# Performance work log

Measured on AMD Instinct MI355X. Metric: run time of the kernel, lower is better.

## Reference

```python
import jax, jax.numpy as jnp
import numpy as np

RATE = 2
KSIZE = 3          # patch size for similarity
KERNEL = 2 * RATE  # patch size for alpha scatter (4)
BN_EPS = 1e-5


def _extract_patches(x, k, s):
    """Mirror of GuidedCxtAtten.extract_patches: reflect-pad then unfold.
    x: [B,C,H,W] -> [B,Ho,Wo,C,k,k] with Ho=H//s, Wo=W//s."""
    left = (k - s + 1) // 2
    right = (k - s) // 2
    xp = jnp.pad(x, ((0, 0), (0, 0), (left, right), (left, right)), mode='reflect')
    Hp, Wp = xp.shape[2], xp.shape[3]
    Ho = (Hp - k) // s + 1
    Wo = (Wp - k) // s + 1
    ii = (jnp.arange(Ho) * s)[:, None] + jnp.arange(k)[None, :]   # [Ho,k]
    jj = (jnp.arange(Wo) * s)[:, None] + jnp.arange(k)[None, :]   # [Wo,k]
    p = xp[:, :, ii[:, :, None, None], jj[None, None, :, :]]      # [B,C,Ho,k,Wo,k]
    return p.transpose(0, 2, 4, 1, 3, 5)                          # [B,Ho,Wo,C,k,k]


def setup_inputs() -> dict:
    key = jax.random.key(0)
    ks = jax.random.split(key, 5)
    B, Cg, Ca, H, W = 4, 256, 128, 128, 128
    f = jax.random.normal(ks[0], (B, Cg, H, W), dtype=jnp.float32)
    alpha = jax.random.normal(ks[1], (B, Ca, H, W), dtype=jnp.float32)
    unknown = (jax.random.uniform(ks[2], (B, 1, H, W)) > 0.5).astype(jnp.float32)
    # guidance_conv: 1x1, Cg -> Cg//2, xavier-ish
    gc_w = jax.random.normal(ks[3], (Cg // 2, Cg), dtype=jnp.float32) * np.sqrt(2.0 / (Cg + Cg // 2))
    gc_b = jnp.zeros((Cg // 2,), dtype=jnp.float32)
    # W[0]: 1x1 conv Ca->Ca no bias; W[1]: BN with gamma=0.001, beta=0 per init
    w_w = jax.random.normal(ks[4], (Ca, Ca), dtype=jnp.float32) * np.sqrt(1.0 / Ca)
    bn_gamma = jnp.full((Ca,), 0.001, dtype=jnp.float32)
    bn_beta = jnp.zeros((Ca,), dtype=jnp.float32)
    return {"f": f, "alpha": alpha, "unknown": unknown, "gc_w": gc_w, "gc_b": gc_b,
            "w_w": w_w, "bn_gamma": bn_gamma, "bn_beta": bn_beta}


def _forward(f, alpha, unknown, gc_w, gc_b, w_w, bn_gamma, bn_beta):
    # guidance 1x1 conv
    fg = jnp.einsum('oi,bihw->bohw', gc_w, f) + gc_b[None, :, None, None]
    B, _, H, W = fg.shape
    Ca = alpha.shape[1]
    Hs, Ws = H // RATE, W // RATE
    L = Hs * Ws

    # alpha patches [B,L,Ca,4,4] (kernel=2*rate, stride=rate)
    alpha_w = _extract_patches(alpha, KERNEL, RATE).reshape(B, L, Ca, KERNEL, KERNEL)

    # nearest downsample by rate (torch nearest with scale 1/2 == strided pick)
    f_ds = fg[:, :, ::RATE, ::RATE]                # [B,Cg/2,Hs,Ws]
    unk_ds = unknown[:, :, ::RATE, ::RATE]         # [B,1,Hs,Ws]

    # similarity filter patches [B,L,C,3,3]
    w = _extract_patches(f_ds, KSIZE, 1).reshape(B, L, -1, KSIZE, KSIZE)

    # known/unknown softmax scales [B,2]
    u_mean = unk_ds.mean(axis=(2, 3))              # [B,1]
    k_mean = 1.0 - u_mean
    su = jnp.clip(jnp.sqrt(u_mean / k_mean), 0.1, 10.0)
    sk = jnp.clip(jnp.sqrt(k_mean / u_mean), 0.1, 10.0)
    softmax_scale = jnp.concatenate([su, sk], axis=1)

    # patch-mean of unknown mask -> binary patch mask [B,L]
    m = _extract_patches(unk_ds, KSIZE, 1).reshape(B, L, -1).mean(axis=2)
    mm = (m > 0.0).astype(fg.dtype)

    # l2-normalize filters per patch, then correlate against all positions.
    # Conv of reflect-padded f_ds with stride-1 3x3 patch filters == inner
    # product of normalized patches with the raw patches (same extraction).
    norm = jnp.sqrt(jnp.sum(w * w, axis=(2, 3, 4), keepdims=True))
    w_normed = w / jnp.maximum(norm, 1e-4)
    scores = jnp.einsum('bqcij,bpcij->bqp', w_normed, w)   # [B,L(q=patch),L(p=pos)]

    # known/unknown scaling per source patch q
    gate = jnp.where(mm > 0.0, su, sk)                      # [B,L]
    scores = scores * gate[:, :, None]

    # self-match suppression only for unknown patches (diagonal q == p)
    diag = jnp.arange(L)
    scores = scores.at[:, diag, diag].add(-10000.0 * mm)

    attn = jax.nn.softmax(scores, axis=1)                   # softmax over patches q

    # offsets (argmax patch per position, relative to center)
    idx = jnp.argmax(attn, axis=1)                          # [B,L]
    offsets = jnp.stack([idx // Ws, idx % Ws], axis=1).reshape(B, 2, Hs, Ws)
    offsets = offsets - jnp.array([Hs // 2, Ws // 2]).reshape(1, 2, 1, 1)

    # scatter alpha patches with attention weights: per-sample conv_transpose2d
    attn_map = attn.reshape(B, L, Hs, Ws)

    def ct(yi, wc):  # yi [L,Hs,Ws], wc [L,Ca,4,4]
        rhs = jnp.flip(wc, (2, 3)).transpose(1, 0, 2, 3)    # [Ca,L,4,4]
        pad = KERNEL - 1 - 1                                # torch padding=1
        out = jax.lax.conv_general_dilated(
            yi[None], rhs, window_strides=(1, 1),
            padding=[(pad, pad), (pad, pad)], lhs_dilation=(RATE, RATE),
            dimension_numbers=('NCHW', 'OIHW', 'NCHW'))
        return out[0]

    y = jax.vmap(ct)(attn_map, alpha_w) / 4.0               # [B,Ca,H,W]

    # W: 1x1 conv (no bias) + BatchNorm2d (training-mode batch stats)
    yw = jnp.einsum('oi,bihw->bohw', w_w, y)
    mean = yw.mean(axis=(0, 2, 3))
    var = yw.var(axis=(0, 2, 3))
    yn = (yw - mean[None, :, None, None]) * jax.lax.rsqrt(var + BN_EPS)[None, :, None, None]
    yn = yn * bn_gamma[None, :, None, None] + bn_beta[None, :, None, None]

    return yn + alpha, offsets, softmax_scale


def reference(f, alpha, unknown, gc_w, gc_b, w_w, bn_gamma, bn_beta):
    return _forward(f, alpha, unknown, gc_w, gc_b, w_w, bn_gamma, bn_beta)
```

## Files before the change

kernel.cpp:

```cpp
#include <hip/hip_runtime.h>
#include <math.h>

#define B 4
#define CG 256
#define CM 128
#define CA 128
#define H 128
#define W_ 128
#define HS 64
#define WS 64
#define L 4096
#define D1 1152
#define D2 2048
#define NPIX 65536
#define NT1 36
#define NT2 128

#define STP_F 8388608UL
#define RA_F  4194304UL
#define SLOT_F (STP_F + RA_F + RA_F)

typedef unsigned short u16;
typedef __attribute__((ext_vector_type(8))) short short8v;
typedef __attribute__((ext_vector_type(4))) unsigned short u16x4;
typedef __attribute__((ext_vector_type(4))) float f32x4;

__device__ __forceinline__ float bf2f(u16 x) {
    union { unsigned int u; float f; } v; v.u = ((unsigned int)x) << 16; return v.f;
}
__device__ __forceinline__ u16 f2bf(float x) {
    union { float f; unsigned int u; } v; v.f = x;
    unsigned int r = (v.u + 0x7FFFu + ((v.u >> 16) & 1u)) >> 16;
    return (u16)r;
}
__device__ __forceinline__ void gll16(const void* g, void* l) {
    __builtin_amdgcn_global_load_lds((const __attribute__((address_space(1))) void*)g,
                                     (__attribute__((address_space(3))) void*)l, 16, 0, 0);
}
__device__ __forceinline__ int refl(int i, int n) {
    return i < 0 ? -i : (i >= n ? 2 * n - 2 - i : i);
}
__device__ __forceinline__ int swz(int row, int fq) {
    return row * 32 + ((fq ^ ((row >> 1) & 3)) * 8);
}
__device__ __forceinline__ short8v rdfrag32(const char* lds, int r, int fq) {
    return *(const short8v*)(lds + r * 64 + ((fq * 16) ^ (((r >> 1) & 3) << 4)));
}

__global__ __launch_bounds__(256) void k_conv_ds(const float* __restrict__ f,
                                                 const float* __restrict__ gw,
                                                 const float* __restrict__ gb,
                                                 float* __restrict__ fds,
                                                 float* __restrict__ ssq) {
    __shared__ float sf[CG * 64];
    __shared__ float part[4][64];
    int t = threadIdx.x;
    int hs = blockIdx.x, b = blockIdx.y;
    const float* fb = f + (size_t)b * CG * H * W_ + (2 * hs) * W_;
    for (int idx = t; idx < CG * 64; idx += 256) {
        int ci = idx >> 6, ws = idx & 63;
        sf[idx] = fb[(size_t)ci * H * W_ + 2 * ws];
    }
    __syncthreads();
    int ws = t & 63;
    int wave = __builtin_amdgcn_readfirstlane(t >> 6);
    const float* gwp = gw + (size_t)(wave * 32) * CG;
    float acc[32];
#pragma unroll
    for (int r = 0; r < 32; ++r) acc[r] = gb[wave * 32 + r];
    for (int ci = 0; ci < CG; ++ci) {
        float fv = sf[ci * 64 + ws];
#pragma unroll
        for (int r = 0; r < 32; ++r) acc[r] += gwp[r * CG + ci] * fv;
    }
    float sq = 0.f;
#pragma unroll
    for (int r = 0; r < 32; ++r) {
        int co = wave * 32 + r;
        fds[(((size_t)b * CM + co) * HS + hs) * WS + ws] = acc[r];
        sq += acc[r] * acc[r];
    }
    part[wave][ws] = sq;
    __syncthreads();
    if (t < 64)
        ssq[((size_t)b * HS + hs) * WS + t] =
            part[0][t] + part[1][t] + part[2][t] + part[3][t];
}

__global__ __launch_bounds__(256) void k_scale(const float* __restrict__ unk,
                                               float* __restrict__ suk,
                                               float* __restrict__ out2) {
    int b = blockIdx.x, t = threadIdx.x;
    __shared__ float red[256];
    float s = 0.f;
    for (int i = t; i < L; i += 256) {
        int hs = i >> 6, ws = i & 63;
        s += unk[(size_t)b * H * W_ + (2 * hs) * W_ + 2 * ws];
    }
    red[t] = s;
    __syncthreads();
    for (int o = 128; o > 0; o >>= 1) {
        if (t < o) red[t] += red[t + o];
        __syncthreads();
    }
    if (t == 0) {
        float u = red[0] / (float)L;
        float k = 1.0f - u;
        float su = sqrtf(u / k); su = fminf(fmaxf(su, 0.1f), 10.0f);
        float sk = sqrtf(k / u); sk = fminf(fmaxf(sk, 0.1f), 10.0f);
        suk[b * 2] = su; suk[b * 2 + 1] = sk;
        out2[b * 2] = su; out2[b * 2 + 1] = sk;
    }
}

__global__ __launch_bounds__(64) void k_gate(const float* __restrict__ unk,
                                             const float* __restrict__ ssq,
                                             const float* __restrict__ suk,
                                             float* __restrict__ g,
                                             float* __restrict__ dg) {
    int ws = threadIdx.x, hs = blockIdx.x, b = blockIdx.y;
    float sm = 0.f, sq = 0.f;
    for (int di = -1; di <= 1; ++di) {
        int rh = refl(hs + di, HS);
        for (int dj = -1; dj <= 1; ++dj) {
            int rw = refl(ws + dj, WS);
            sm += unk[(size_t)b * H * W_ + (2 * rh) * W_ + 2 * rw];
            sq += ssq[((size_t)b * HS + rh) * WS + rw];
        }
    }
    float mm   = (sm > 0.0f) ? 1.0f : 0.0f;
    float norm = sqrtf(sq);
    float gate = (mm > 0.0f) ? suk[2 * b] : suk[2 * b + 1];
    int q = hs * WS + ws;
    g[(size_t)b * L + q]  = gate / fmaxf(norm, 1e-4f);
    dg[(size_t)b * L + q] = -10000.0f * mm;
}

__global__ __launch_bounds__(256) void k_buildW(const float* __restrict__ fds,
                                                float* __restrict__ base, int b0) {
    int bz = blockIdx.z;
    int b  = b0 + bz;
    u16* Whi = (u16*)(base + (size_t)bz * SLOT_F + STP_F);
    int ws = threadIdx.x;
    int c  = blockIdx.y * 4 + threadIdx.y;
    int hs = blockIdx.x;
    int q = hs * WS + ws;
    size_t bo = (size_t)q * D1 + c * 9;
    const float* src = fds + ((size_t)b * CM + c) * HS * WS;
#pragma unroll
    for (int i = 0; i < 3; ++i) {
        int rh = refl(hs + i - 1, HS);
#pragma unroll
        for (int j = 0; j < 3; ++j) {
            int rw = refl(ws + j - 1, WS);
            Whi[bo + i * 3 + j] = f2bf(src[rh * WS + rw]);
        }
    }
}

__global__ __launch_bounds__(256, 3) void k_gemm1(float* __restrict__ base,
                                                  const float* __restrict__ g0,
                                                  const float* __restrict__ dg0,
                                                  int b0) {
    __shared__ u16 sA[3][128 * 32], sB[3][128 * 32];
    int bz = blockIdx.z;
    float* S = base + (size_t)bz * SLOT_F;
    u16* STP = (u16*)S;
    const u16* Whi = (const u16*)(S + STP_F);
    const float* g  = g0  + (size_t)(b0 + bz) * L;
    const float* dg = dg0 + (size_t)(b0 + bz) * L;

    int tid = threadIdx.x;
    int wv = tid >> 6, lane = tid & 63;
    int t0 = blockIdx.x, I = 0;
    while (t0 >= 32 - I) { t0 -= 32 - I; ++I; }
    int J = I + t0;
    int pTile = I * 128, qTile = J * 128;
    int wp = (wv >> 1) * 64, wq = (wv & 1) * 64;
    int r0 = wv * 32;
    int lrow = lane >> 2;
    int csw = ((lane & 3) ^ ((lrow >> 1) & 3)) * 8;
    int fr = lane & 15, fq = lane >> 4;

    const u16* gArow = Whi + (size_t)(pTile + r0 + lrow) * D1 + csw;
    const u16* gBrow = Whi + (size_t)(qTile + r0 + lrow) * D1 + csw;

#define G1STG(kt, bf) do { \
    gll16(gArow + (kt) * 32, &sA[bf][r0 * 32]); \
    gll16(gArow + (kt) * 32 + (size_t)16 * D1, &sA[bf][(r0 + 16) * 32]); \
    gll16(gBrow + (kt) * 32, &sB[bf][r0 * 32]); \
    gll16(gBrow + (kt) * 32 + (size_t)16 * D1, &sB[bf][(r0 + 16) * 32]); } while (0)

#define G1PHASE(t, ca, cb, na, nb_) do { \
    int nxb = ((t) + 1) % 3; \
    _Pragma("unroll") for (int i = 0; i < 4; ++i) \
        nb_[i] = *(const short8v*)&sB[nxb][swz(wq + i * 16 + fr, fq)]; \
    __builtin_amdgcn_s_setprio(1); \
    _Pragma("unroll") for (int mi = 0; mi < 2; ++mi) \
        _Pragma("unroll") for (int ni = 0; ni < 4; ++ni) \
            acc[mi][ni] = __builtin_amdgcn_mfma_f32_16x16x32_bf16(ca[mi], cb[ni], acc[mi][ni], 0, 0, 0); \
    __builtin_amdgcn_s_setprio(0); \
    _Pragma("unroll") for (int i = 0; i < 4; ++i) \
        na[i] = *(const short8v*)&sA[nxb][swz(wp + i * 16 + fr, fq)]; \
    G1STG(((t) + 3 < NT1) ? (t) + 3 : 0, (t) % 3); \
    asm volatile("s_waitcnt vmcnt(4)" ::: "memory"); \
    __builtin_amdgcn_s_setprio(1); \
    _Pragma("unroll") for (int mi = 2; mi < 4; ++mi) \
        _Pragma("unroll") for (int ni = 0; ni < 4; ++ni) \
            acc[mi][ni] = __builtin_amdgcn_mfma_f32_16x16x32_bf16(ca[mi], cb[ni], acc[mi][ni], 0, 0, 0); \
    __builtin_amdgcn_s_setprio(0); \
    asm volatile("s_waitcnt lgkmcnt(0)" ::: "memory"); \
    __builtin_amdgcn_s_barrier(); \
    __builtin_amdgcn_sched_barrier(0); } while (0)

    f32x4 acc[4][4];
#pragma unroll
    for (int mi = 0; mi < 4; ++mi)
#pragma unroll
        for (int ni = 0; ni < 4; ++ni)
#pragma unroll
            for (int r = 0; r < 4; ++r) acc[mi][ni][r] = 0.f;

    G1STG(0, 0);
    G1STG(1, 1);
    G1STG(2, 2);
    asm volatile("s_waitcnt vmcnt(4)" ::: "memory");
    __builtin_amdgcn_s_barrier();
    __builtin_amdgcn_sched_barrier(0);

    short8v fa0[4], fb0[4], fa1[4], fb1[4];
#pragma unroll
    for (int i = 0; i < 4; ++i) {
        fa0[i] = *(const short8v*)&sA[0][swz(wp + i * 16 + fr, fq)];
        fb0[i] = *(const short8v*)&sB[0][swz(wq + i * 16 + fr, fq)];
    }
    asm volatile("s_waitcnt lgkmcnt(0)" ::: "memory");
    __builtin_amdgcn_s_barrier();
    __builtin_amdgcn_sched_barrier(0);

    for (int t = 0; t < NT1; t += 2) {
        G1PHASE(t,     fa0, fb0, fa1, fb1);
        G1PHASE(t + 1, fa1, fb1, fa0, fb0);
    }
#undef G1PHASE
#undef G1STG

#pragma unroll
    for (int ni = 0; ni < 4; ++ni) {
        int qq = qTile + wq + ni * 16 + fr;
        float gq = g[qq];
        float dq = dg[qq];
#pragma unroll
        for (int mi = 0; mi < 4; ++mi) {
            int pB = pTile + wp + mi * 16 + fq * 4;
#pragma unroll
            for (int r = 0; r < 4; ++r) {
                int p = pB + r;
                float v = acc[mi][ni][r] * gq;
                if (p == qq) v += dq;
                STP[(size_t)p * L + qq] = f2bf(v);
            }
        }
    }
    if (I != J) {
#pragma unroll
        for (int mi = 0; mi < 4; ++mi) {
            int p0 = pTile + wp + mi * 16 + fq * 4;
            float gp0 = g[p0], gp1 = g[p0 + 1], gp2 = g[p0 + 2], gp3 = g[p0 + 3];
#pragma unroll
            for (int ni = 0; ni < 4; ++ni) {
                int qq = qTile + wq + ni * 16 + fr;
                u16x4 mv;
                mv[0] = f2bf(acc[mi][ni][0] * gp0);
                mv[1] = f2bf(acc[mi][ni][1] * gp1);
                mv[2] = f2bf(acc[mi][ni][2] * gp2);
                mv[3] = f2bf(acc[mi][ni][3] * gp3);
                *(u16x4*)(STP + (size_t)qq * L + p0) = mv;
            }
        }
    }
}

__global__ __launch_bounds__(256) void k_softmax(float* __restrict__ base,
                                                 const float* __restrict__ fds,
                                                 const float* __restrict__ g0,
                                                 const float* __restrict__ dg0,
                                                 float* __restrict__ rowsum,
                                                 float* __restrict__ out1, int b0) {
    __shared__ float wmax[4], wsum[4], cred[4];
    __shared__ int candList[128];
    __shared__ int candCount;
    int bz = blockIdx.y;
    int b  = b0 + bz;
    float* S = base + (size_t)bz * SLOT_F;
    u16* STP = (u16*)S;
    const float* fdsb = fds + (size_t)b * CM * HS * WS;
    const float* g  = g0  + (size_t)b * L;
    const float* dg = dg0 + (size_t)b * L;

    int p = blockIdx.x, t = threadIdx.x;
    int lane = t & 63, wv = t >> 6;
    u16* rowp = STP + (size_t)p * L;

    if (t == 0) candCount = 0;
    float mx = -3.4e38f;
    for (int i = t; i < L / 8; i += 256) {
        short8v v8 = ((const short8v*)rowp)[i];
#pragma unroll
        for (int j = 0; j < 8; ++j) mx = fmaxf(mx, bf2f((u16)v8[j]));
    }
#pragma unroll
    for (int o = 32; o > 0; o >>= 1) mx = fmaxf(mx, __shfl_xor(mx, o));
    if (lane == 0) wmax[wv] = mx;
    __syncthreads();
    float M = fmaxf(fmaxf(wmax[0], wmax[1]), fmaxf(wmax[2], wmax[3]));
    float cth = M - (fabsf(M) * 0.0625f + 1e-5f);

    float s = 0.f;
    for (int i = t; i < L / 8; i += 256) {
        short8v v8 = ((const short8v*)rowp)[i];
        short8v o8;
#pragma unroll
        for (int j = 0; j < 8; ++j) {
            float v = bf2f((u16)v8[j]);
            if (v >= cth) {
                int ix = atomicAdd(&candCount, 1);
                if (ix < 128) candList[ix] = i * 8 + j;
            }
            float e = __expf(v - M);
            o8[j] = (short)f2bf(e);
            s += e;
        }
        ((short8v*)rowp)[i] = o8;
    }
#pragma unroll
    for (int o = 32; o > 0; o >>= 1) s += __shfl_xor(s, o);
    if (lane == 0) wsum[wv] = s;
    __syncthreads();
    if (t == 0) rowsum[(size_t)b * L + p] = wsum[0] + wsum[1] + wsum[2] + wsum[3];

    int nc = candCount; if (nc > 128) nc = 128;
    int bestI;
    if (nc == 1) {
        bestI = candList[0];
    } else {
        float bestE = -3.4e38f; bestI = L;
        int hp = p >> 6, wpp = p & 63;
        for (int k = 0; k < nc; ++k) {
            int cand = candList[k];
            int hc = cand >> 6, wcc = cand & 63;
            float part = 0.f;
#pragma unroll
            for (int e = 0; e < 5; ++e) {
                int kk = t + e * 256;
                if (kk < D1) {
                    int c  = kk / 9, ij = kk - c * 9;
                    int di = ij / 3, dj = ij - di * 3;
                    float pv = fdsb[(size_t)c * (HS * WS)
                                    + refl(hp + di - 1, HS) * WS + refl(wpp + dj - 1, WS)];
                    float cv = fdsb[(size_t)c * (HS * WS)
                                    + refl(hc + di - 1, HS) * WS + refl(wcc + dj - 1, WS)];
                    part += pv * cv;
                }
            }
#pragma unroll
            for (int o = 32; o > 0; o >>= 1) part += __shfl_xor(part, o);
            if (lane == 0) cred[wv] = part;
            __syncthreads();
            float e1 = (cred[0] + cred[1] + cred[2] + cred[3]) * g[cand]
                     + (p == cand ? dg[cand] : 0.f);
            if (e1 > bestE || (e1 == bestE && cand < bestI)) { bestE = e1; bestI = cand; }
            __syncthreads();
        }
    }
    if (t == 0) {
        out1[(size_t)(b * 2 + 0) * L + p] = (float)(bestI / WS - 32);
        out1[(size_t)(b * 2 + 1) * L + p] = (float)(bestI % WS - 32);
    }
}

__global__ __launch_bounds__(256) void k_buildA(const float* __restrict__ alpha,
                                                float* __restrict__ base, int b0) {
    int bz = blockIdx.z;
    int b  = b0 + bz;
    u16* At = (u16*)(base + (size_t)bz * SLOT_F + STP_F);
    int q0 = (blockIdx.x * 256 + threadIdx.x) * 4;
    int n  = blockIdx.y;
    int c = n & 127, kikj = n >> 7, ki = kikj >> 2, kj = kikj & 3;
    int hs = q0 >> 6, ws = q0 & 63;
    int rh = refl(2 * hs + ki - 1, H);
    const float* arow = alpha + ((size_t)b * CA + c) * H * W_ + rh * W_;
    u16x4 ov;
#pragma unroll
    for (int j = 0; j < 4; ++j)
        ov[j] = f2bf(arow[refl(2 * (ws + j) + kj - 1, W_)]);
    *(u16x4*)(At + (size_t)n * L + q0) = ov;
}

__global__ __launch_bounds__(512, 2) void k_gemm2(float* __restrict__ base) {
    __shared__ u16 smem[65536];
    char* sm = (char*)smem;
    int bz = blockIdx.z;
    float* S = base + (size_t)bz * SLOT_F;
    const u16* P  = (const u16*)S;
    const u16* At = (const u16*)(S + STP_F);
    u16* Z        = (u16*)(S + STP_F + RA_F);

    int tid = threadIdx.x;
    int wid = tid >> 6, lane = tid & 63;
    int wm = wid >> 2, wn = wid & 3;
    int pTile = blockIdx.x * 256, nTile = blockIdx.y * 256;
    int fr = lane & 15, fq = lane >> 4;

    int off0 = wid * 1024 + lane * 16;
    int row0 = off0 >> 6, cb0 = off0 & 63;
    int off1 = off0 + 8192;
    int row1 = off1 >> 6, cb1 = off1 & 63;
    const u16* pA0 = P  + (size_t)(pTile + row0) * L + ((cb0 ^ (((row0 >> 1) & 3) << 4)) >> 1);
    const u16* pA1 = P  + (size_t)(pTile + row1) * L + ((cb1 ^ (((row1 >> 1) & 3) << 4)) >> 1);
    const u16* pB0 = At + (size_t)(nTile + row0) * L + ((cb0 ^ (((row0 >> 1) & 3) << 4)) >> 1);
    const u16* pB1 = At + (size_t)(nTile + row1) * L + ((cb1 ^ (((row1 >> 1) & 3) << 4)) >> 1);

#define STG2(kt, bi) do { \
    char* d = sm + (bi) * 32768 + wid * 1024; \
    gll16(pA0 + (size_t)(kt) * 32, d); \
    gll16(pA1 + (size_t)(kt) * 32, d + 8192); \
    gll16(pB0 + (size_t)(kt) * 32, d + 16384); \
    gll16(pB1 + (size_t)(kt) * 32, d + 24576); } while (0)

#define PRELOAD2(fa, fb, bi) do { \
    const char* Ab_ = sm + (bi) * 32768; \
    const char* Bb_ = Ab_ + 16384; \
    _Pragma("unroll") for (int n = 0; n < 4; ++n) fb[n] = rdfrag32(Bb_, wn * 64 + n * 16 + fr, fq); \
    _Pragma("unroll") for (int m = 0; m < 8; ++m) fa[m] = rdfrag32(Ab_, wm * 128 + m * 16 + fr, fq); } while (0)

#define PHASE2(t, ca, cb, na, nb_) do { \
    const char* Abn = sm + (((t) + 1) & 3) * 32768; \
    const char* Bbn = Abn + 16384; \
    _Pragma("unroll") for (int n = 0; n < 4; ++n) nb_[n] = rdfrag32(Bbn, wn * 64 + n * 16 + fr, fq); \
    __builtin_amdgcn_s_setprio(1); \
    _Pragma("unroll") for (int m = 0; m < 4; ++m) \
        _Pragma("unroll") for (int n = 0; n < 4; ++n) \
            acc[m][n] = __builtin_amdgcn_mfma_f32_16x16x32_bf16(ca[m], cb[n], acc[m][n], 0, 0, 0); \
    __builtin_amdgcn_s_setprio(0); \
    _Pragma("unroll") for (int m = 0; m < 8; ++m) na[m] = rdfrag32(Abn, wm * 128 + m * 16 + fr, fq); \
    STG2(((t) + 3 < NT2) ? (t) + 3 : 0, ((t) + 3) & 3); \
    asm volatile("s_waitcnt vmcnt(4)" ::: "memory"); \
    __builtin_amdgcn_s_setprio(1); \
    _Pragma("unroll") for (int m = 4; m < 8; ++m) \
        _Pragma("unroll") for (int n = 0; n < 4; ++n) \
            acc[m][n] = __builtin_amdgcn_mfma_f32_16x16x32_bf16(ca[m], cb[n], acc[m][n], 0, 0, 0); \
    __builtin_amdgcn_s_setprio(0); \
    asm volatile("s_waitcnt lgkmcnt(0)" ::: "memory"); \
    __builtin_amdgcn_s_barrier(); \
    __builtin_amdgcn_sched_barrier(0); } while (0)

    f32x4 acc[8][4];
#pragma unroll
    for (int m = 0; m < 8; ++m)
#pragma unroll
        for (int n = 0; n < 4; ++n)
#pragma unroll
            for (int r = 0; r < 4; ++r) acc[m][n][r] = 0.f;

    STG2(0, 0);
    STG2(1, 1);
    STG2(2, 2);
    asm volatile("s_waitcnt vmcnt(4)" ::: "memory");
    __builtin_amdgcn_s_barrier();
    __builtin_amdgcn_sched_barrier(0);

    short8v fa0[8], fb0[4], fa1[8], fb1[4];
    PRELOAD2(fa0, fb0, 0);
    asm volatile("s_waitcnt lgkmcnt(0)" ::: "memory");
    __builtin_amdgcn_s_barrier();
    __builtin_amdgcn_sched_barrier(0);

    for (int t = 0; t < NT2; t += 2) {
        PHASE2(t,     fa0, fb0, fa1, fb1);
        PHASE2(t + 1, fa1, fb1, fa0, fb0);
    }
#undef PHASE2
#undef PRELOAD2
#undef STG2

#pragma unroll
    for (int m = 0; m < 8; ++m)
#pragma unroll
        for (int n = 0; n < 4; ++n) {
            int nn = nTile + wn * 64 + n * 16 + fr;
#pragma unroll
            for (int r = 0; r < 4; ++r) {
                int pp = pTile + wm * 128 + m * 16 + fq * 4 + r;
                Z[(size_t)pp * D2 + nn] = f2bf(acc[m][n][r]);
            }
        }
}

__global__ __launch_bounds__(256) void k_gather(float* __restrict__ base,
                                                const float* __restrict__ rowsum,
                                                u16* __restrict__ yt, int b0) {
    int bz = blockIdx.z;
    int b  = b0 + bz;
    const u16* Z = (const u16*)(base + (size_t)bz * SLOT_F + STP_F + RA_F);
    const float* rs = rowsum + (size_t)b * L;
    int c  = threadIdx.x & 127;
    int pl = threadIdx.x >> 7;
    int w  = blockIdx.x * 2 + pl;
    int h  = blockIdx.y;
    float s = 0.f;
#pragma unroll
    for (int ki = 0; ki < 4; ++ki) {
        int num = h + 1 - ki;
        if (num < 0 || (num & 1)) continue;
        int hs = num >> 1;
        if (hs >= HS) continue;
#pragma unroll
        for (int kj = 0; kj < 4; ++kj) {
            int numw = w + 1 - kj;
            if (numw < 0 || (numw & 1)) continue;
            int wsd = numw >> 1;
            if (wsd >= WS) continue;
            int src = hs * WS + wsd;
            s += bf2f(Z[(size_t)src * D2 + (ki * 4 + kj) * 128 + c]) / rs[src];
        }
    }
    int pix = h * W_ + w;
    int cs = c ^ ((pix & 7) << 3);
    yt[((size_t)b * 16384 + pix) * 128 + cs] = f2bf(0.25f * s);
}

__global__ __launch_bounds__(256) void k_cvtww(const float* __restrict__ ww,
                                               u16* __restrict__ wwbf) {
    int i = blockIdx.x * 256 + threadIdx.x;
    int o = i >> 7, c = i & 127;
    wwbf[o * 128 + (c ^ ((o & 7) << 3))] = f2bf(ww[i]);
}

__global__ __launch_bounds__(256) void k_ywgemm(const u16* __restrict__ wwbf,
                                                const u16* __restrict__ yt,
                                                float* __restrict__ yw) {
    __shared__ u16 sA[128 * 128], sB[128 * 128];
    int tid = threadIdx.x;
    int wv = tid >> 6, lane = tid & 63;
    int nTile = blockIdx.x * 128;
    int wp = (wv >> 1) * 64, wn = (wv & 1) * 64;
    int fr = lane & 15, fq = lane >> 4;

    const u16* gB = yt + (size_t)nTile * 128;
#pragma unroll
    for (int i = 0; i < 8; ++i) {
        int o = (i * 4 + wv) * 512;
        gll16(wwbf + o + lane * 8, &sA[o]);
        gll16(gB + o + lane * 8, &sB[o]);
    }
    __syncthreads();

    f32x4 acc[4][4];
#pragma unroll
    for (int mi = 0; mi < 4; ++mi)
#pragma unroll
        for (int ni = 0; ni < 4; ++ni)
#pragma unroll
            for (int r = 0; r < 4; ++r) acc[mi][ni][r] = 0.f;

#pragma unroll
    for (int ks = 0; ks < 4; ++ks) {
        int k0 = ks * 32 + fq * 8;
        short8v a[4], bb[4];
#pragma unroll
        for (int i = 0; i < 4; ++i) {
            int ra = wp + i * 16 + fr;
            a[i] = *(const short8v*)&sA[ra * 128 + (k0 ^ ((ra & 7) << 3))];
            int rb = wn + i * 16 + fr;
            bb[i] = *(const short8v*)&sB[rb * 128 + (k0 ^ ((rb & 7) << 3))];
        }
#pragma unroll
        for (int mi = 0; mi < 4; ++mi)
#pragma unroll
            for (int ni = 0; ni < 4; ++ni)
                acc[mi][ni] = __builtin_amdgcn_mfma_f32_16x16x32_bf16(a[mi], bb[ni], acc[mi][ni], 0, 0, 0);
    }

#pragma unroll
    for (int mi = 0; mi < 4; ++mi)
#pragma unroll
        for (int ni = 0; ni < 4; ++ni) {
            int gp = nTile + wn + ni * 16 + fr;
#pragma unroll
            for (int r = 0; r < 4; ++r) {
                int o = wp + mi * 16 + fq * 4 + r;
                yw[(size_t)o * NPIX + gp] = acc[mi][ni][r];
            }
        }
}

__global__ __launch_bounds__(256) void k_stats(const float* __restrict__ yw,
                                               float* __restrict__ meanvar) {
    int o = blockIdx.x, t = threadIdx.x;
    __shared__ float rs[256], rq[256];
    float s = 0.f, q = 0.f;
    const float* p = yw + (size_t)o * NPIX;
    for (int i = t; i < NPIX; i += 256) {
        float v = p[i];
        s += v;
        q += v * v;
    }
    rs[t] = s; rq[t] = q;
    __syncthreads();
    for (int off = 128; off > 0; off >>= 1) {
        if (t < off) { rs[t] += rs[t + off]; rq[t] += rq[t + off]; }
        __syncthreads();
    }
    if (t == 0) {
        float n = (float)NPIX;
        float mean = rs[0] / n;
        float var  = rq[0] / n - mean * mean;
        meanvar[o] = mean;
        meanvar[CA + o] = var;
    }
}

__global__ __launch_bounds__(256) void k_final(const float* __restrict__ yw,
                                               const float* __restrict__ meanvar,
                                               const float* __restrict__ gamma,
                                               const float* __restrict__ beta,
                                               const float* __restrict__ alpha,
                                               float* __restrict__ out0) {
    size_t i = ((size_t)blockIdx.x * 256 + threadIdx.x) * 4;
    int c = (int)((i >> 14) & 127);
    int b = (int)(i >> 21);
    int pix = (int)(i & 16383);
    float4 v = *(const float4*)(yw + (size_t)c * NPIX + b * 16384 + pix);
    float4 a = *(const float4*)(alpha + i);
    float mean = meanvar[c];
    float var  = meanvar[CA + c];
    float sc   = rsqrtf(var + 1e-5f) * gamma[c];
    float bt   = beta[c];
    float4 r;
    r.x = (v.x - mean) * sc + bt + a.x;
    r.y = (v.y - mean) * sc + bt + a.y;
    r.z = (v.z - mean) * sc + bt + a.z;
    r.w = (v.w - mean) * sc + bt + a.w;
    *(float4*)(out0 + i) = r;
}

extern "C" void kernel_launch(void* const* d_in, const int* in_sizes, int n_in,
                              void* d_out, int out_size, void* d_ws, size_t ws_size,
                              hipStream_t stream) {
    (void)in_sizes; (void)n_in; (void)out_size;
    const float* f     = (const float*)d_in[0];
    const float* alpha = (const float*)d_in[1];
    const float* unk   = (const float*)d_in[2];
    const float* gw    = (const float*)d_in[3];
    const float* gb    = (const float*)d_in[4];
    const float* ww    = (const float*)d_in[5];
    const float* gamma = (const float*)d_in[6];
    const float* beta  = (const float*)d_in[7];

    float* out0 = (float*)d_out;
    float* out1 = out0 + (size_t)B * CA * H * W_;
    float* out2 = out1 + (size_t)B * 2 * HS * WS;

    float* wsf = (float*)d_ws;
    size_t off = 0;
    float* fds     = wsf + off; off += (size_t)B * CM * HS * WS;
    float* ssq     = wsf + off; off += (size_t)B * HS * WS;
    float* gbuf    = wsf + off; off += (size_t)B * L;
    float* dgbuf   = wsf + off; off += (size_t)B * L;
    float* suk     = wsf + off; off += 64;
    float* ytF     = wsf + off; off += (size_t)NPIX * 128 / 2;
    float* wwbfF   = wsf + off; off += 8192;
    float* meanvar = wsf + off; off += 256;
    float* rowsum  = wsf + off; off += (size_t)B * L;
    float* base    = wsf + off;

    const size_t PRE_F = off;
    int nb = (ws_size >= (PRE_F + 4 * SLOT_F) * sizeof(float)) ? 4 : 2;

    float* yw   = base;
    u16*   yt   = (u16*)ytF;
    u16*   wwbf = (u16*)wwbfF;

    k_cvtww<<<64, 256, 0, stream>>>(ww, wwbf);
    k_conv_ds<<<dim3(64, 4), 256, 0, stream>>>(f, gw, gb, fds, ssq);
    k_scale<<<4, 256, 0, stream>>>(unk, suk, out2);
    k_gate<<<dim3(64, 4), 64, 0, stream>>>(unk, ssq, suk, gbuf, dgbuf);

    for (int b0 = 0; b0 < B; b0 += nb) {
        k_buildW<<<dim3(64, 32, nb), dim3(64, 4), 0, stream>>>(fds, base, b0);
        k_gemm1<<<dim3(528, 1, nb), 256, 0, stream>>>(base, gbuf, dgbuf, b0);
        k_softmax<<<dim3(4096, nb), 256, 0, stream>>>(base, fds, gbuf, dgbuf, rowsum, out1, b0);
        k_buildA<<<dim3(4, 2048, nb), 256, 0, stream>>>(alpha, base, b0);
        k_gemm2<<<dim3(16, 8, nb), 512, 0, stream>>>(base);
        k_gather<<<dim3(64, 128, nb), 256, 0, stream>>>(base, rowsum, yt, b0);
    }

    k_ywgemm<<<512, 256, 0, stream>>>(wwbf, yt, yw);
    k_stats<<<128, 256, 0, stream>>>(yw, meanvar);
    k_final<<<8192, 256, 0, stream>>>(yw, meanvar, gamma, beta, alpha, out0);
}
```

Measured before the change: 803.7 us.

## Map one softmax row per wavefront and keep row in registers

The softmax/argmax kernel now gives each 64-lane wavefront its own row, so four rows run per block instead of one row per 256-thread block. Each lane loads its eight 16-byte chunks into registers once and reuses them for both the max pass and the exp pass, instead of reading global memory twice. All block-level __syncthreads and shared reductions, including those in the candidate-refinement loop, become wave-local shuffles. This raises register use and caps candidates per row at 64 instead of 128, which could change the argmax if more than 64 near-max candidates occur.

```diff
diff --git a/kernel.cpp b/kernel.cpp
--- a/kernel.cpp
+++ b/kernel.cpp
@@ -287,9 +287,8 @@
                                                  const float* __restrict__ dg0,
                                                  float* __restrict__ rowsum,
                                                  float* __restrict__ out1, int b0) {
-    __shared__ float wmax[4], wsum[4], cred[4];
-    __shared__ int candList[128];
-    __shared__ int candCount;
+    __shared__ int candList[4][64];
+    __shared__ int candCount[4];
     int bz = blockIdx.y;
     int b  = b0 + bz;
     float* S = base + (size_t)bz * SLOT_F;
@@ -298,82 +297,76 @@
     const float* g  = g0  + (size_t)b * L;
     const float* dg = dg0 + (size_t)b * L;
 
-    int p = blockIdx.x, t = threadIdx.x;
+    int t = threadIdx.x;
     int lane = t & 63, wv = t >> 6;
+    int p = blockIdx.x * 4 + wv;
     u16* rowp = STP + (size_t)p * L;
-
-    if (t == 0) candCount = 0;
+    if (lane == 0) candCount[wv] = 0;
+
+    short8v v[8];
+#pragma unroll
+    for (int j = 0; j < 8; ++j) v[j] = ((const short8v*)rowp)[j * 64 + lane];
+
     float mx = -3.4e38f;
-    for (int i = t; i < L / 8; i += 256) {
-        short8v v8 = ((const short8v*)rowp)[i];
-#pragma unroll
-        for (int j = 0; j < 8; ++j) mx = fmaxf(mx, bf2f((u16)v8[j]));
-    }
+#pragma unroll
+    for (int j = 0; j < 8; ++j)
+#pragma unroll
+        for (int jj = 0; jj < 8; ++jj) mx = fmaxf(mx, bf2f((u16)v[j][jj]));
 #pragma unroll
     for (int o = 32; o > 0; o >>= 1) mx = fmaxf(mx, __shfl_xor(mx, o));
-    if (lane == 0) wmax[wv] = mx;
-    __syncthreads();
-    float M = fmaxf(fmaxf(wmax[0], wmax[1]), fmaxf(wmax[2], wmax[3]));
+    float M = mx;
     float cth = M - (fabsf(M) * 0.0625f + 1e-5f);
 
     float s = 0.f;
-    for (int i = t; i < L / 8; i += 256) {
-        short8v v8 = ((const short8v*)rowp)[i];
+#pragma unroll
+    for (int j = 0; j < 8; ++j) {
         short8v o8;
 #pragma unroll
-        for (int j = 0; j < 8; ++j) {
-            float v = bf2f((u16)v8[j]);
-            if (v >= cth) {
-                int ix = atomicAdd(&candCount, 1);
-                if (ix < 128) candList[ix] = i * 8 + j;
+        for (int jj = 0; jj < 8; ++jj) {
+            float x = bf2f((u16)v[j][jj]);
+            if (x >= cth) {
+                int ix = atomicAdd(&candCount[wv], 1);
+                if (ix < 64) candList[wv][ix] = (j * 64 + lane) * 8 + jj;
             }
-            float e = __expf(v - M);
-            o8[j] = (short)f2bf(e);
+            float e = __expf(x - M);
+            o8[jj] = (short)f2bf(e);
             s += e;
         }
-        ((short8v*)rowp)[i] = o8;
+        ((short8v*)rowp)[j * 64 + lane] = o8;
     }
 #pragma unroll
     for (int o = 32; o > 0; o >>= 1) s += __shfl_xor(s, o);
-    if (lane == 0) wsum[wv] = s;
-    __syncthreads();
-    if (t == 0) rowsum[(size_t)b * L + p] = wsum[0] + wsum[1] + wsum[2] + wsum[3];
-
-    int nc = candCount; if (nc > 128) nc = 128;
+    if (lane == 0) rowsum[(size_t)b * L + p] = s;
+
+    int nc = candCount[wv]; if (nc > 64) nc = 64;
     int bestI;
     if (nc == 1) {
-        bestI = candList[0];
+        bestI = candList[wv][0];
     } else {
         float bestE = -3.4e38f; bestI = L;
         int hp = p >> 6, wpp = p & 63;
         for (int k = 0; k < nc; ++k) {
-            int cand = candList[k];
+            int cand = candList[wv][k];
             int hc = cand >> 6, wcc = cand & 63;
             float part = 0.f;
 #pragma unroll
-            for (int e = 0; e < 5; ++e) {
-                int kk = t + e * 256;
-                if (kk < D1) {
-                    int c  = kk / 9, ij = kk - c * 9;
-                    int di = ij / 3, dj = ij - di * 3;
-                    float pv = fdsb[(size_t)c * (HS * WS)
-                                    + refl(hp + di - 1, HS) * WS + refl(wpp + dj - 1, WS)];
-                    float cv = fdsb[(size_t)c * (HS * WS)
-                                    + refl(hc + di - 1, HS) * WS + refl(wcc + dj - 1, WS)];
-                    part += pv * cv;
-                }
+            for (int e = 0; e < 18; ++e) {
+                int kk = lane + e * 64;
+                int c  = kk / 9, ij = kk - c * 9;
+                int di = ij / 3, dj = ij - di * 3;
+                float pv = fdsb[(size_t)c * (HS * WS)
+                                + refl(hp + di - 1, HS) * WS + refl(wpp + dj - 1, WS)];
+                float cv = fdsb[(size_t)c * (HS * WS)
+                                + refl(hc + di - 1, HS) * WS + refl(wcc + dj - 1, WS)];
+                part += pv * cv;
             }
 #pragma unroll
             for (int o = 32; o > 0; o >>= 1) part += __shfl_xor(part, o);
-            if (lane == 0) cred[wv] = part;
-            __syncthreads();
-            float e1 = (cred[0] + cred[1] + cred[2] + cred[3]) * g[cand]
-                     + (p == cand ? dg[cand] : 0.f);
+            float e1 = part * g[cand] + (p == cand ? dg[cand] : 0.f);
             if (e1 > bestE || (e1 == bestE && cand < bestI)) { bestE = e1; bestI = cand; }
-            __syncthreads();
-        }
-    }
-    if (t == 0) {
+        }
+    }
+    if (lane == 0) {
         out1[(size_t)(b * 2 + 0) * L + p] = (float)(bestI / WS - 32);
         out1[(size_t)(b * 2 + 1) * L + p] = (float)(bestI % WS - 32);
     }
@@ -690,7 +683,7 @@
     for (int b0 = 0; b0 < B; b0 += nb) {
         k_buildW<<<dim3(64, 32, nb), dim3(64, 4), 0, stream>>>(fds, base, b0);
         k_gemm1<<<dim3(528, 1, nb), 256, 0, stream>>>(base, gbuf, dgbuf, b0);
-        k_softmax<<<dim3(4096, nb), 256, 0, stream>>>(base, fds, gbuf, dgbuf, rowsum, out1, b0);
+        k_softmax<<<dim3(1024, nb), 256, 0, stream>>>(base, fds, gbuf, dgbuf, rowsum, out1, b0);
         k_buildA<<<dim3(4, 2048, nb), 256, 0, stream>>>(alpha, base, b0);
         k_gemm2<<<dim3(16, 8, nb), 512, 0, stream>>>(base);
         k_gather<<<dim3(64, 128, nb), 256, 0, stream>>>(base, rowsum, yt, b0);
```

After: 828.3 us. 1.03x slower.
